# Optimization experiments

Measured on AMD Instinct MI355X. Metric: run time of the kernel, lower is better.

Reference implementation:

```python
import jax, jax.numpy as jnp
import numpy as np

B, S, D, H = 4, 2048, 1024, 16
DH = D // H
NEG = -10000.0


def setup_inputs() -> dict:
    key = jax.random.key(0)
    ks = jax.random.split(key, 12)
    scale = 0.02
    inp = {
        "q": jax.random.normal(ks[0], (B, S, D), jnp.float32),
        "k": jax.random.normal(ks[1], (B, S, D), jnp.float32),
        "v": jax.random.normal(ks[2], (B, S, D), jnp.float32),
        "mask": jnp.triu(jnp.ones((S, S), jnp.bool_), k=1),  # True = masked (causal)
        "Wq": jax.random.normal(ks[3], (D, D), jnp.float32) * scale,
        "bq": jnp.zeros((D,), jnp.float32),
        "Wk": jax.random.normal(ks[4], (D, D), jnp.float32) * scale,
        "bk": jnp.zeros((D,), jnp.float32),
        "Wv": jax.random.normal(ks[5], (D, D), jnp.float32) * scale,
        "bv": jnp.zeros((D,), jnp.float32),
        "Wo": jax.random.normal(ks[6], (D, D), jnp.float32) * scale,
        "bo": jnp.zeros((D,), jnp.float32),
    }
    return inp


def _split(x):
    # [B,S,D] -> [B,H,S,DH]
    return x.reshape(B, S, H, DH).transpose(0, 2, 1, 3)


def reference(q, k, v, mask, Wq, bq, Wk, bk, Wv, bv, Wo, bo):
    # torch Linear: y = x @ W.T + b
    qh = _split(q @ Wq.T + bq)
    kh = _split(k @ Wk.T + bk)
    vh = _split(v @ Wv.T + bv)
    # scaled dot-product scores: [B,H,S,S]
    scores = jnp.einsum("bhqd,bhkd->bhqk", qh, kh) / jnp.sqrt(jnp.float32(DH))
    scores = scores + jnp.where(mask, jnp.float32(NEG), jnp.float32(0.0))
    attn = jax.nn.softmax(scores, axis=-1)  # dropout_rate=0 -> identity
    out = jnp.einsum("bhqk,bhkd->bhqd", attn, vh)
    out = out.transpose(0, 2, 1, 3).reshape(B, S, D)
    return out @ Wo.T + bo
```

## Files before the change

### kernel.cpp

```cpp
#include <hip/hip_runtime.h>
#include <hip/hip_bf16.h>


#define B_ 4
#define S_ 2048
#define D_ 1024
#define H_ 16
#define DH_ 64
#define M_ (B_*S_)
#define MASKADD (-14427.0f)
#define QSCALE  (0.180336880f)

typedef __attribute__((ext_vector_type(8)))  __bf16 bf16x8;
typedef __attribute__((ext_vector_type(8)))  unsigned short ushort8;
typedef __attribute__((ext_vector_type(4)))  float f32x4;
typedef __attribute__((ext_vector_type(16))) float f32x16;

__device__ __forceinline__ unsigned short f2bf(float f) {
  __hip_bfloat16 h = __float2bfloat16(f);
  union { __hip_bfloat16 h; unsigned short u; } c; c.h = h; return c.u;
}

__device__ __forceinline__ f32x4 mfma16(bf16x8 a, bf16x8 b, f32x4 c) {
  return __builtin_amdgcn_mfma_f32_16x16x32_bf16(a, b, c, 0, 0, 0);
}
__device__ __forceinline__ f32x16 mfma32(bf16x8 a, bf16x8 b, f32x16 c) {
  return __builtin_amdgcn_mfma_f32_32x32x16_bf16(a, b, c, 0, 0, 0);
}

__device__ __forceinline__ unsigned cvtpk(float lo, float hi) {
  unsigned r;
  asm("v_cvt_pk_bf16_f32 %0, %1, %2" : "=v"(r) : "v"(lo), "v"(hi));
  return r;
}

__device__ __forceinline__ void gld_lds16(const void* g, void* l) {
  __builtin_amdgcn_global_load_lds(
      (const __attribute__((address_space(1))) unsigned int*)g,
      (__attribute__((address_space(3))) unsigned int*)l, 16, 0, 0);
}

__global__ void cvt4_kernel(const float* __restrict__ p0, const float* __restrict__ p1,
                            const float* __restrict__ p2, const float* __restrict__ p3,
                            unsigned short* __restrict__ o0, unsigned short* __restrict__ o1,
                            unsigned short* __restrict__ o2, unsigned short* __restrict__ o3,
                            int n4) {
  int i = blockIdx.x * blockDim.x + threadIdx.x;
  if (i >= n4) return;
  const float* in  = (blockIdx.y == 0) ? p0 : (blockIdx.y == 1 ? p1 : (blockIdx.y == 2 ? p2 : p3));
  unsigned short* out = (blockIdx.y == 0) ? o0 : (blockIdx.y == 1 ? o1 : (blockIdx.y == 2 ? o2 : o3));
  float4 f = reinterpret_cast<const float4*>(in)[i];
  ushort4 o;
  o.x = f2bf(f.x); o.y = f2bf(f.y); o.z = f2bf(f.z); o.w = f2bf(f.w);
  reinterpret_cast<ushort4*>(out)[i] = o;
}

template<bool F32A>
__device__ __forceinline__
void gemm_body(const void* __restrict__ Ap, const unsigned short* __restrict__ W,
               const float* __restrict__ bias, void* __restrict__ outp,
               int mode, bool sc,
               unsigned short* sA16, float* sA32, unsigned short* sB)
{
  const int tid  = threadIdx.x;
  const int lane = tid & 63, wid = tid >> 6;
  const int bx = blockIdx.x;
  const int j8 = bx & 7, i8 = bx >> 3;
  const int mt = j8*8 + (i8 >> 3), nt = i8 & 7;
  const int m0 = mt*128, n0 = nt*128;
  const int wr = wid >> 1, wc = wid & 1;
  const int g = lane >> 4;

  const float* A32 = (const float*)Ap;
  const unsigned short* A16 = (const unsigned short*)Ap;

  f32x4 acc[4][4];
  #pragma unroll
  for (int i = 0; i < 4; ++i)
    #pragma unroll
    for (int j = 0; j < 4; ++j)
      #pragma unroll
      for (int r = 0; r < 4; ++r) acc[i][j][r] = 0.0f;

  auto stageB = [&](int bufi, int kt) {
    const unsigned short* Wb = W + (size_t)n0*D_ + kt*32;
    #pragma unroll
    for (int p = 0; p < 2; ++p) {
      int r = 32*wid + 16*p + (lane >> 2);
      int c = (lane & 3) * 8;
      gld_lds16(Wb + (size_t)r*D_ + c, &sB[bufi*4096 + (32*wid + 16*p)*32]);
    }
  };
  auto stageA16 = [&](int bufi, int kt) {
    const unsigned short* Ab = A16 + (size_t)m0*D_ + kt*32;
    #pragma unroll
    for (int p = 0; p < 2; ++p) {
      int r = 32*wid + 16*p + (lane >> 2);
      int c = (lane & 3) * 8;
      gld_lds16(Ab + (size_t)r*D_ + c, &sA16[bufi*4096 + (32*wid + 16*p)*32]);
    }
  };
  auto stageA32 = [&](int bufi, int kt) {
    const float* Ab = A32 + (size_t)m0*D_ + kt*32;
    #pragma unroll
    for (int p = 0; p < 4; ++p) {
      int ch = 4*wid + p;
      int row = ch*8 + (lane >> 3);
      int cbs = ((lane & 7) * 16) ^ ((lane >> 3) << 4);
      gld_lds16(Ab + (size_t)row*D_ + (cbs >> 2), &sA32[bufi*4096 + ch*256]);
    }
  };

  if (F32A) stageA32(0, 0); else stageA16(0, 0);
  stageB(0, 0);

  const int NK = D_/32;
  int buf = 0;
  for (int kt = 0; kt < NK; ++kt) {
    __syncthreads();
    if (kt + 1 < NK) {
      if (F32A) stageA32(buf ^ 1, kt + 1);
      else      stageA16(buf ^ 1, kt + 1);
      stageB(buf ^ 1, kt + 1);
    }

    bf16x8 aF[4], bF[4];
    #pragma unroll
    for (int i = 0; i < 4; ++i) {
      int row = 64*wr + 16*i + (lane & 15);
      if (F32A) {
        const char* base = (const char*)(sA32 + buf*4096) + row*128;
        int sw = (row & 7) << 4;
        f32x4 a0 = *(const f32x4*)(base + ((g*32)      ^ sw));
        f32x4 a1 = *(const f32x4*)(base + ((g*32 + 16) ^ sw));
        union { unsigned u[4]; bf16x8 v; } af;
        af.u[0] = cvtpk(a0[0], a0[1]);
        af.u[1] = cvtpk(a0[2], a0[3]);
        af.u[2] = cvtpk(a1[0], a1[1]);
        af.u[3] = cvtpk(a1[2], a1[3]);
        aF[i] = af.v;
      } else {
        aF[i] = *(const bf16x8*)&sA16[buf*4096 + row*32 + g*8];
      }
    }
    #pragma unroll
    for (int j = 0; j < 4; ++j)
      bF[j] = *(const bf16x8*)&sB[buf*4096 + (64*wc + 16*j + (lane & 15))*32 + g*8];

    #pragma unroll
    for (int i = 0; i < 4; ++i)
      #pragma unroll
      for (int j = 0; j < 4; ++j)
        acc[i][j] = mfma16(aF[i], bF[j], acc[i][j]);
    buf ^= 1;
  }

  #pragma unroll
  for (int i = 0; i < 4; ++i) {
    int gr0 = m0 + 64*wr + 16*i + ((lane >> 4) << 2);
    #pragma unroll
    for (int j = 0; j < 4; ++j) {
      int gc = n0 + 64*wc + 16*j + (lane & 15);
      float bv = bias[gc];
      if (mode == 2) {
        int b = gr0 >> 11, s = gr0 & (S_ - 1);
        int hh = gc >> 6, dh = gc & (DH_ - 1);
        ushort4 o;
        o.x = f2bf(acc[i][j][0] + bv); o.y = f2bf(acc[i][j][1] + bv);
        o.z = f2bf(acc[i][j][2] + bv); o.w = f2bf(acc[i][j][3] + bv);
        *(ushort4*)&((unsigned short*)outp)[(((size_t)b*H_ + hh)*DH_ + dh)*S_ + s] = o;
      } else {
        #pragma unroll
        for (int r = 0; r < 4; ++r) {
          float v = acc[i][j][r] + bv;
          if (sc) v *= QSCALE;
          int gr = gr0 + r;
          if (mode == 0) {
            int b = gr >> 11, s = gr & (S_ - 1);
            int hh = gc >> 6, dh = gc & (DH_ - 1);
            ((unsigned short*)outp)[(((size_t)b*H_ + hh)*S_ + s)*DH_ + dh] = f2bf(v);
          } else {
            ((float*)outp)[(size_t)gr*D_ + gc] = v;
          }
        }
      }
    }
  }
}

__global__ __launch_bounds__(256, 3)
void gemm_qkv(const float* __restrict__ Aq, const float* __restrict__ Ak,
              const float* __restrict__ Av,
              const unsigned short* __restrict__ Wq_, const unsigned short* __restrict__ Wk_,
              const unsigned short* __restrict__ Wv_,
              const float* __restrict__ bq_, const float* __restrict__ bk_,
              const float* __restrict__ bv_,
              unsigned short* __restrict__ Oq, unsigned short* __restrict__ Ok,
              unsigned short* __restrict__ Ov)
{
  __shared__ float          sA32[2*4096];
  __shared__ unsigned short sB  [2*4096];
  const int y = blockIdx.y;
  const float* A = (y == 0) ? Aq : (y == 1 ? Ak : Av);
  const unsigned short* W = (y == 0) ? Wq_ : (y == 1 ? Wk_ : Wv_);
  const float* bias        = (y == 0) ? bq_ : (y == 1 ? bk_ : bv_);
  unsigned short* outp     = (y == 0) ? Oq  : (y == 1 ? Ok  : Ov);
  gemm_body<true>(A, W, bias, outp, (y == 2) ? 2 : 0, y == 0, nullptr, sA32, sB);
}

__global__ __launch_bounds__(256, 3)
void gemm_out(const unsigned short* __restrict__ A, const unsigned short* __restrict__ W,
              const float* __restrict__ bias, float* __restrict__ outp)
{
  __shared__ unsigned short sA16[2*4096];
  __shared__ unsigned short sB  [2*4096];
  gemm_body<false>(A, W, bias, outp, 1, false, sA16, nullptr, sB);
}

__global__ __launch_bounds__(256)
void attn_kernel(const unsigned short* __restrict__ Qh, const unsigned short* __restrict__ Kh,
                 const unsigned short* __restrict__ Vt, unsigned short* __restrict__ AO)
{
  __shared__ unsigned short sK [2][64*64];
  __shared__ unsigned short sVt[2][64*64];

  const int tid = threadIdx.x, lane = tid & 63, wid = tid >> 6;
  const int l31 = lane & 31, h5 = lane >> 5;
  const int bh = blockIdx.x;
  const int by = blockIdx.y;
  const int bb = bh >> 4, hd = bh & 15;
  const unsigned short* Qb = Qh + (size_t)bh * S_ * DH_;
  const unsigned short* Kb = Kh + (size_t)bh * S_ * DH_;
  const unsigned short* Vb = Vt + (size_t)bh * DH_ * S_;

  auto stageK = [&](int bufi, int t) {
    #pragma unroll
    for (int p = 0; p < 2; ++p) {
      int ch = 2*wid + p;
      int row = ch*8 + (lane >> 3);
      int cbs = ((lane & 7) * 16) ^ ((row & 7) << 4);
      gld_lds16(Kb + (size_t)(t*64 + row)*DH_ + (cbs >> 1), &sK[bufi][ch*512]);
    }
  };
  auto stageV = [&](int bufi, int t) {
    #pragma unroll
    for (int p = 0; p < 2; ++p) {
      int ch = 2*wid + p;
      int row = ch*8 + (lane >> 3);
      int cbs = ((lane & 7) * 16) ^ ((row & 7) << 4);
      gld_lds16(Vb + (size_t)row*S_ + t*64 + (cbs >> 1), &sVt[bufi][ch*512]);
    }
  };

  f32x16 zz;
  #pragma unroll
  for (int r = 0; r < 16; ++r) zz[r] = 0.0f;

  for (int ci = 0; ci < 2; ++ci) {
    const int chunk = ci ? by : 15 - by;
    const int qc0 = chunk * 128;
    const int NT  = 2*chunk + 2;
    const int qw0 = qc0 + wid*32;
    const int q   = qw0 + l31;

    bf16x8 qF[4];
    #pragma unroll
    for (int c = 0; c < 4; ++c)
      qF[c] = *(const bf16x8*)(Qb + (size_t)q*DH_ + c*16 + h5*8);

    f32x16 accO0 = zz, accO1 = zz;
    float lsum = 0.0f;

    __syncthreads();
    stageK(0, 0);
    stageV(0, 0);

    int buf = 0;
    for (int t = 0; t < NT; ++t) {
      __syncthreads();
      if (t + 1 < NT) { stageK(buf ^ 1, t + 1); stageV(buf ^ 1, t + 1); }

      #pragma unroll
      for (int sub = 0; sub < 2; ++sub) {
        const int kv0 = t*64 + sub*32;
        if (kv0 > qw0 + 31) continue;
        const bool dodiag = (kv0 + 31 > qw0);

        f32x16 st = zz;
        __builtin_amdgcn_s_setprio(1);
        #pragma unroll
        for (int c = 0; c < 4; ++c) {
          int row = sub*32 + l31;
          const char* base = (const char*)&sK[buf][0] + row*128;
          bf16x8 kf = *(const bf16x8*)(base + ((32*c + 16*h5) ^ ((row & 7) << 4)));
          st = mfma32(kf, qF[c], st);
        }
        __builtin_amdgcn_s_setprio(0);

        #pragma unroll
        for (int r = 0; r < 16; ++r) {
          float x = st[r];
          if (dodiag) {
            int kv = kv0 + (r & 3) + 8*(r >> 2) + 4*h5;
            if (kv > q) x += MASKADD;
          }
          x = __builtin_amdgcn_exp2f(x);
          st[r] = x;
          lsum += x;
        }

        #pragma unroll
        for (int hh = 0; hh < 2; ++hh) {
          union { unsigned u[4]; bf16x8 v; } pb;
          pb.u[0] = cvtpk(st[8*hh+0], st[8*hh+1]);
          pb.u[1] = cvtpk(st[8*hh+2], st[8*hh+3]);
          pb.u[2] = cvtpk(st[8*hh+4], st[8*hh+5]);
          pb.u[3] = cvtpk(st[8*hh+6], st[8*hh+7]);

          __builtin_amdgcn_s_setprio(1);
          #pragma unroll
          for (int dh = 0; dh < 2; ++dh) {
            int row = dh*32 + l31;
            const char* base = (const char*)&sVt[buf][0] + row*128;
            int sw = (row & 7) << 4;
            int X = 64*sub + 32*hh + 8*h5;
            union { uint2 g[2]; bf16x8 v; } vv;
            vv.g[0] = *(const uint2*)(base + ((X)      ^ sw));
            vv.g[1] = *(const uint2*)(base + ((X + 16) ^ sw));
            if (dh == 0) accO0 = mfma32(vv.v, pb.v, accO0);
            else         accO1 = mfma32(vv.v, pb.v, accO1);
          }
          __builtin_amdgcn_s_setprio(0);
        }
      }
      buf ^= 1;
    }

    float lt = lsum + __shfl_xor(lsum, 32, 64);
    float inv = 1.0f / lt;
    unsigned short* ao = AO + ((size_t)bb*S_ + q)*D_ + hd*DH_;
    #pragma unroll
    for (int dh = 0; dh < 2; ++dh) {
      const f32x16 A = dh ? accO1 : accO0;
      #pragma unroll
      for (int rq = 0; rq < 4; ++rq) {
        ushort4 o;
        o.x = f2bf(A[4*rq+0] * inv);
        o.y = f2bf(A[4*rq+1] * inv);
        o.z = f2bf(A[4*rq+2] * inv);
        o.w = f2bf(A[4*rq+3] * inv);
        int dbase = dh*32 + 8*rq + 4*h5;
        *(ushort4*)&ao[dbase] = o;
      }
    }
  }
}

extern "C" void kernel_launch(void* const* d_in, const int* in_sizes, int n_in,
                              void* d_out, int out_size, void* d_ws, size_t ws_size,
                              hipStream_t stream)
{
  const float* q  = (const float*)d_in[0];
  const float* k  = (const float*)d_in[1];
  const float* v  = (const float*)d_in[2];
  const float* Wq = (const float*)d_in[4];
  const float* bq = (const float*)d_in[5];
  const float* Wk = (const float*)d_in[6];
  const float* bk = (const float*)d_in[7];
  const float* Wv = (const float*)d_in[8];
  const float* bv = (const float*)d_in[9];
  const float* Wo = (const float*)d_in[10];
  const float* bo = (const float*)d_in[11];

  unsigned short* ws = (unsigned short*)d_ws;
  const size_t MD = (size_t)M_ * D_;
  const size_t DD = (size_t)D_ * D_;
  unsigned short* Wqb = ws;
  unsigned short* Wkb = Wqb + DD;
  unsigned short* Wvb = Wkb + DD;
  unsigned short* Wob = Wvb + DD;
  unsigned short* Qhb = Wob + DD;
  unsigned short* Khb = Qhb + MD;
  unsigned short* Vtb = Khb + MD;
  unsigned short* AOb = Vtb + MD;

  cvt4_kernel<<<dim3((int)(DD/4/256), 4), 256, 0, stream>>>(Wq, Wk, Wv, Wo, Wqb, Wkb, Wvb, Wob, (int)(DD/4));

  gemm_qkv<<<dim3(512, 3), 256, 0, stream>>>(q, k, v, Wqb, Wkb, Wvb,
                                             bq, bk, bv, Qhb, Khb, Vtb);

  attn_kernel<<<dim3(64, 8), 256, 0, stream>>>(Qhb, Khb, Vtb, AOb);

  gemm_out<<<512, 256, 0, stream>>>(AOb, Wob, bo, (float*)d_out);
}
```

Measured before the change: 181.6 us.

## Split long causal attention chunks across KV halves with separate combine kernel

Replaces the paired-chunk scheduling (each block handling chunks 15-by and by) with a grid of 24 per head. The eight longest query chunks are split into two KV ranges whose unnormalized partial outputs and row sums go to fp32 workspace, and the short chunks run whole. A new combine kernel sums the two partials and normalizes into bf16 output. This aims to raise block count and balance the causal workload, but adds an extra launch plus about 32 MB of fp32 partial traffic.

```diff
diff --git a/kernel.cpp b/kernel.cpp
--- a/kernel.cpp
+++ b/kernel.cpp
@@ -219,7 +219,8 @@
 
 __global__ __launch_bounds__(256)
 void attn_kernel(const unsigned short* __restrict__ Qh, const unsigned short* __restrict__ Kh,
-                 const unsigned short* __restrict__ Vt, unsigned short* __restrict__ AO)
+                 const unsigned short* __restrict__ Vt, unsigned short* __restrict__ AO,
+                 float* __restrict__ OP, float* __restrict__ LP)
 {
   __shared__ unsigned short sK [2][64*64];
   __shared__ unsigned short sVt[2][64*64];
@@ -229,9 +230,40 @@
   const int bh = blockIdx.x;
   const int by = blockIdx.y;
   const int bb = bh >> 4, hd = bh & 15;
+
+  int c, t0, t1, half;
+  bool split;
+  if (by < 16) {
+    split = true;
+    c = 15 - (by >> 1);
+    half = by & 1;
+    t0 = half ? (c + 1) : 0;
+    t1 = half ? (2*c + 2) : (c + 1);
+  } else {
+    split = false;
+    c = 7 - (by - 16);
+    half = 0;
+    t0 = 0;
+    t1 = 2*c + 2;
+  }
+
   const unsigned short* Qb = Qh + (size_t)bh * S_ * DH_;
   const unsigned short* Kb = Kh + (size_t)bh * S_ * DH_;
   const unsigned short* Vb = Vt + (size_t)bh * DH_ * S_;
+  const int qc0 = c * 128;
+  const int qw0 = qc0 + wid*32;
+  const int q   = qw0 + l31;
+
+  bf16x8 qF[4];
+  #pragma unroll
+  for (int cc = 0; cc < 4; ++cc)
+    qF[cc] = *(const bf16x8*)(Qb + (size_t)q*DH_ + cc*16 + h5*8);
+
+  f32x16 zz;
+  #pragma unroll
+  for (int r = 0; r < 16; ++r) zz[r] = 0.0f;
+  f32x16 accO0 = zz, accO1 = zz;
+  float lsum = 0.0f;
 
   auto stageK = [&](int bufi, int t) {
     #pragma unroll
@@ -252,91 +284,88 @@
     }
   };
 
-  f32x16 zz;
-  #pragma unroll
-  for (int r = 0; r < 16; ++r) zz[r] = 0.0f;
-
-  for (int ci = 0; ci < 2; ++ci) {
-    const int chunk = ci ? by : 15 - by;
-    const int qc0 = chunk * 128;
-    const int NT  = 2*chunk + 2;
-    const int qw0 = qc0 + wid*32;
-    const int q   = qw0 + l31;
-
-    bf16x8 qF[4];
-    #pragma unroll
-    for (int c = 0; c < 4; ++c)
-      qF[c] = *(const bf16x8*)(Qb + (size_t)q*DH_ + c*16 + h5*8);
-
-    f32x16 accO0 = zz, accO1 = zz;
-    float lsum = 0.0f;
-
+  stageK(0, t0);
+  stageV(0, t0);
+
+  int buf = 0;
+  for (int t = t0; t < t1; ++t) {
     __syncthreads();
-    stageK(0, 0);
-    stageV(0, 0);
-
-    int buf = 0;
-    for (int t = 0; t < NT; ++t) {
-      __syncthreads();
-      if (t + 1 < NT) { stageK(buf ^ 1, t + 1); stageV(buf ^ 1, t + 1); }
-
-      #pragma unroll
-      for (int sub = 0; sub < 2; ++sub) {
-        const int kv0 = t*64 + sub*32;
-        if (kv0 > qw0 + 31) continue;
-        const bool dodiag = (kv0 + 31 > qw0);
-
-        f32x16 st = zz;
+    if (t + 1 < t1) { stageK(buf ^ 1, t + 1); stageV(buf ^ 1, t + 1); }
+
+    #pragma unroll
+    for (int sub = 0; sub < 2; ++sub) {
+      const int kv0 = t*64 + sub*32;
+      if (kv0 > qw0 + 31) continue;
+      const bool dodiag = (kv0 + 31 > qw0);
+
+      f32x16 st = zz;
+      __builtin_amdgcn_s_setprio(1);
+      #pragma unroll
+      for (int cc = 0; cc < 4; ++cc) {
+        int row = sub*32 + l31;
+        const char* base = (const char*)&sK[buf][0] + row*128;
+        bf16x8 kf = *(const bf16x8*)(base + ((32*cc + 16*h5) ^ ((row & 7) << 4)));
+        st = mfma32(kf, qF[cc], st);
+      }
+      __builtin_amdgcn_s_setprio(0);
+
+      #pragma unroll
+      for (int r = 0; r < 16; ++r) {
+        float x = st[r];
+        if (dodiag) {
+          int kv = kv0 + (r & 3) + 8*(r >> 2) + 4*h5;
+          if (kv > q) x += MASKADD;
+        }
+        x = __builtin_amdgcn_exp2f(x);
+        st[r] = x;
+        lsum += x;
+      }
+
+      #pragma unroll
+      for (int hh = 0; hh < 2; ++hh) {
+        union { unsigned u[4]; bf16x8 v; } pb;
+        pb.u[0] = cvtpk(st[8*hh+0], st[8*hh+1]);
+        pb.u[1] = cvtpk(st[8*hh+2], st[8*hh+3]);
+        pb.u[2] = cvtpk(st[8*hh+4], st[8*hh+5]);
+        pb.u[3] = cvtpk(st[8*hh+6], st[8*hh+7]);
+
         __builtin_amdgcn_s_setprio(1);
         #pragma unroll
-        for (int c = 0; c < 4; ++c) {
-          int row = sub*32 + l31;
-          const char* base = (const char*)&sK[buf][0] + row*128;
-          bf16x8 kf = *(const bf16x8*)(base + ((32*c + 16*h5) ^ ((row & 7) << 4)));
-          st = mfma32(kf, qF[c], st);
+        for (int dh = 0; dh < 2; ++dh) {
+          int row = dh*32 + l31;
+          const char* base = (const char*)&sVt[buf][0] + row*128;
+          int sw = (row & 7) << 4;
+          int X = 64*sub + 32*hh + 8*h5;
+          union { uint2 g[2]; bf16x8 v; } vv;
+          vv.g[0] = *(const uint2*)(base + ((X)      ^ sw));
+          vv.g[1] = *(const uint2*)(base + ((X + 16) ^ sw));
+          if (dh == 0) accO0 = mfma32(vv.v, pb.v, accO0);
+          else         accO1 = mfma32(vv.v, pb.v, accO1);
         }
         __builtin_amdgcn_s_setprio(0);
-
-        #pragma unroll
-        for (int r = 0; r < 16; ++r) {
-          float x = st[r];
-          if (dodiag) {
-            int kv = kv0 + (r & 3) + 8*(r >> 2) + 4*h5;
-            if (kv > q) x += MASKADD;
-          }
-          x = __builtin_amdgcn_exp2f(x);
-          st[r] = x;
-          lsum += x;
-        }
-
-        #pragma unroll
-        for (int hh = 0; hh < 2; ++hh) {
-          union { unsigned u[4]; bf16x8 v; } pb;
-          pb.u[0] = cvtpk(st[8*hh+0], st[8*hh+1]);
-          pb.u[1] = cvtpk(st[8*hh+2], st[8*hh+3]);
-          pb.u[2] = cvtpk(st[8*hh+4], st[8*hh+5]);
-          pb.u[3] = cvtpk(st[8*hh+6], st[8*hh+7]);
-
-          __builtin_amdgcn_s_setprio(1);
-          #pragma unroll
-          for (int dh = 0; dh < 2; ++dh) {
-            int row = dh*32 + l31;
-            const char* base = (const char*)&sVt[buf][0] + row*128;
-            int sw = (row & 7) << 4;
-            int X = 64*sub + 32*hh + 8*h5;
-            union { uint2 g[2]; bf16x8 v; } vv;
-            vv.g[0] = *(const uint2*)(base + ((X)      ^ sw));
-            vv.g[1] = *(const uint2*)(base + ((X + 16) ^ sw));
-            if (dh == 0) accO0 = mfma32(vv.v, pb.v, accO0);
-            else         accO1 = mfma32(vv.v, pb.v, accO1);
-          }
-          __builtin_amdgcn_s_setprio(0);
-        }
-      }
-      buf ^= 1;
-    }
-
-    float lt = lsum + __shfl_xor(lsum, 32, 64);
+      }
+    }
+    buf ^= 1;
+  }
+
+  float lt = lsum + __shfl_xor(lsum, 32, 64);
+  if (split) {
+    const int p = (bh*8 + (c - 8))*2 + half;
+    float* Op = OP + (size_t)p * (128*64);
+    const int lrow = wid*32 + l31;
+    if (h5 == 0) LP[p*128 + lrow] = lt;
+    #pragma unroll
+    for (int dh = 0; dh < 2; ++dh) {
+      const f32x16 A = dh ? accO1 : accO0;
+      #pragma unroll
+      for (int rq = 0; rq < 4; ++rq) {
+        float4 o4;
+        o4.x = A[4*rq+0]; o4.y = A[4*rq+1]; o4.z = A[4*rq+2]; o4.w = A[4*rq+3];
+        int dbase = dh*32 + 8*rq + 4*h5;
+        *(float4*)&Op[(size_t)lrow*64 + dbase] = o4;
+      }
+    }
+  } else {
     float inv = 1.0f / lt;
     unsigned short* ao = AO + ((size_t)bb*S_ + q)*D_ + hd*DH_;
     #pragma unroll
@@ -354,6 +383,30 @@
       }
     }
   }
+}
+
+__global__ __launch_bounds__(256)
+void combine_kernel(const float* __restrict__ OP, const float* __restrict__ LP,
+                    unsigned short* __restrict__ AO)
+{
+  int gid = blockIdx.x * 256 + threadIdx.x;
+  int row = gid >> 4, f4 = gid & 15;
+  int bhc = row >> 7, lrow = row & 127;
+  int bh = bhc >> 3, c = (bhc & 7) + 8;
+  const float* O0 = OP + ((size_t)(bhc*2)) * (128*64) + (size_t)lrow*64 + f4*4;
+  const float* O1 = O0 + 128*64;
+  float l = LP[bhc*2*128 + lrow] + LP[(bhc*2 + 1)*128 + lrow];
+  float inv = 1.0f / l;
+  float4 a = *(const float4*)O0;
+  float4 b = *(const float4*)O1;
+  ushort4 o;
+  o.x = f2bf((a.x + b.x) * inv);
+  o.y = f2bf((a.y + b.y) * inv);
+  o.z = f2bf((a.z + b.z) * inv);
+  o.w = f2bf((a.w + b.w) * inv);
+  int bb = bh >> 4, hd = bh & 15;
+  int srow = c*128 + lrow;
+  *(ushort4*)&AO[((size_t)bb*S_ + srow)*D_ + hd*DH_ + f4*4] = o;
 }
 
 extern "C" void kernel_launch(void* const* d_in, const int* in_sizes, int n_in,
@@ -383,13 +436,16 @@
   unsigned short* Khb = Qhb + MD;
   unsigned short* Vtb = Khb + MD;
   unsigned short* AOb = Vtb + MD;
+  float* OP = (float*)(AOb + MD);
+  float* LP = OP + (size_t)1024 * 128 * 64;
 
   cvt4_kernel<<<dim3((int)(DD/4/256), 4), 256, 0, stream>>>(Wq, Wk, Wv, Wo, Wqb, Wkb, Wvb, Wob, (int)(DD/4));
 
   gemm_qkv<<<dim3(512, 3), 256, 0, stream>>>(q, k, v, Wqb, Wkb, Wvb,
                                              bq, bk, bv, Qhb, Khb, Vtb);
 
-  attn_kernel<<<dim3(64, 8), 256, 0, stream>>>(Qhb, Khb, Vtb, AOb);
+  attn_kernel<<<dim3(64, 24), 256, 0, stream>>>(Qhb, Khb, Vtb, AOb, OP, LP);
+  combine_kernel<<<4096, 256, 0, stream>>>(OP, LP, AOb);
 
   gemm_out<<<512, 256, 0, stream>>>(AOb, Wob, bo, (float*)d_out);
 }
```

New measurement: 211.1 us. 16.2% more time.
